# Optimization experiments

Hardware: AMD Instinct MI355X
Metric: run time of the kernel (lower is better)

## Reference

```python
import jax, jax.numpy as jnp
import numpy as np

D_MODEL = 1024
N_HEADS = 16
HEAD_DIM = D_MODEL // N_HEADS
WINDOW = 512


def _rope(q, k, seq_len, head_dim):
    # interleaved RoPE, identical to the torch implementation
    theta = 1.0 / 10000.0 ** (jnp.arange(0, head_dim, 2, dtype=jnp.float32) / head_dim)
    pos = jnp.arange(seq_len, dtype=jnp.float32)
    freqs = jnp.outer(pos, theta)                      # [S, hD/2]
    cos_f = jnp.cos(freqs)[None, None]                 # [1,1,S,hD/2]
    sin_f = jnp.sin(freqs)[None, None]

    def rotate(x):
        x1, x2 = x[..., ::2], x[..., 1::2]
        return jnp.stack([x1 * cos_f - x2 * sin_f, x1 * sin_f + x2 * cos_f], axis=-1).reshape(x.shape)

    return rotate(q), rotate(k)


def _sliding_window_attn(q, k, v, W, scale):
    # chunked O(S*W) causal sliding-window attention
    B, nH, S, hD = q.shape
    n_chunks = (S + W - 1) // W
    pad_s = n_chunks * W - S
    k_pad = jnp.pad(k, ((0, 0), (0, 0), (W, pad_s), (0, 0)))
    v_pad = jnp.pad(v, ((0, 0), (0, 0), (W, pad_s), (0, 0)))
    q_pad = jnp.pad(q, ((0, 0), (0, 0), (0, pad_s), (0, 0)))
    q_c = q_pad.reshape(B, nH, n_chunks, W, hD)
    k_r = k_pad.reshape(B, nH, n_chunks + 1, W, hD)
    v_r = v_pad.reshape(B, nH, n_chunks + 1, W, hD)
    # window i = chunks [i, i+1] of the left-padded sequence (== torch unfold)
    k_c = jnp.concatenate([k_r[:, :, :-1], k_r[:, :, 1:]], axis=3)  # [B,nH,C,2W,hD]
    v_c = jnp.concatenate([v_r[:, :, :-1], v_r[:, :, 1:]], axis=3)
    attn = jnp.einsum('bhcqd,bhckd->bhcqk', q_c, k_c) * scale

    qi = jnp.arange(W)[:, None]
    ki = jnp.arange(2 * W)[None, :]
    cw_mask = (ki <= qi) | (ki > qi + W)               # [W, 2W]
    chunk_idx = jnp.arange(n_chunks)[:, None]
    abs_k = chunk_idx * W + ki - W                     # [C, 2W]
    pad_mask = (abs_k < 0) | (abs_k >= S)
    q_pos = jnp.arange(n_chunks * W).reshape(n_chunks, W)
    full_mask = cw_mask[None] | pad_mask[:, None, :] | (q_pos >= S)[..., None]  # [C,W,2W]

    attn = jnp.where(full_mask[None, None], -jnp.inf, attn)
    attn = jax.nn.softmax(attn, axis=-1)
    attn = jnp.nan_to_num(attn, nan=0.0)
    out = jnp.einsum('bhcqk,bhckd->bhcqd', attn, v_c)
    return out.reshape(B, nH, n_chunks * W, hD)[:, :, :S]


def _rmsnorm(x, w):
    eps = jnp.finfo(x.dtype).eps
    return x * jax.lax.rsqrt(jnp.mean(x * x, axis=-1, keepdims=True) + eps) * w


def _sdpa(q, k, v, scale):
    s = jnp.einsum('bhqd,bhkd->bhqk', q, k) * scale
    return jnp.einsum('bhqk,bhkd->bhqd', jax.nn.softmax(s, axis=-1), v)


def setup_inputs() -> dict:
    key = jax.random.key(0)
    ks = jax.random.split(key, 11)
    D = D_MODEL
    std = 0.02
    return {
        'x': jax.random.normal(ks[0], (2, 4096, D), jnp.float32),
        'landmarks': jax.random.normal(ks[1], (2, 256, D), jnp.float32),
        'archived_landmarks': jax.random.normal(ks[2], (2, 128, D), jnp.float32),
        'W_qkv': jax.random.normal(ks[3], (D, 3 * D), jnp.float32) * std,
        'W_lm': jax.random.normal(ks[4], (D, 2 * D), jnp.float32) * std,
        'W_arch': jax.random.normal(ks[5], (D, 2 * D), jnp.float32) * std,
        'W_o': jax.random.normal(ks[6], (D, D), jnp.float32) * std,
        'W_gate': jax.random.normal(ks[7], (3 * D, 2 * D), jnp.float32) * std,
        'g_local': jnp.ones((D,), jnp.float32),
        'g_lm': jnp.ones((D,), jnp.float32),
        'g_arch': jnp.ones((D,), jnp.float32),
    }


def reference(x, landmarks, archived_landmarks, W_qkv, W_lm, W_arch, W_o, W_gate, g_local, g_lm, g_arch):
    B, S, D = x.shape
    nH, hD = N_HEADS, HEAD_DIM
    scale = hD ** -0.5

    def rsh(t, L):
        return jnp.transpose(t.reshape(B, L, nH, hD), (0, 2, 1, 3))

    q, k, v = jnp.split(x @ W_qkv, 3, axis=-1)
    Q, K, V = rsh(q, S), rsh(k, S), rsh(v, S)
    Q, K = _rope(Q, K, S, hD)

    Weff = min(WINDOW, S)
    out_loc = _sliding_window_attn(Q, K, V, Weff, scale)  # S > Weff -> chunked path
    out_loc = _rmsnorm(jnp.transpose(out_loc, (0, 2, 1, 3)).reshape(B, S, D), g_local)

    L = landmarks.shape[1]
    K_lm, V_lm = jnp.split(landmarks @ W_lm, 2, axis=-1)
    out_lm = _sdpa(Q, rsh(K_lm, L), rsh(V_lm, L), scale)
    out_lm = _rmsnorm(jnp.transpose(out_lm, (0, 2, 1, 3)).reshape(B, S, D), g_lm)

    A = archived_landmarks.shape[1]
    K_a, V_a = jnp.split(archived_landmarks @ W_arch, 2, axis=-1)
    out_a = _sdpa(Q, rsh(K_a, A), rsh(V_a, A), scale)
    out_a = _rmsnorm(jnp.transpose(out_a, (0, 2, 1, 3)).reshape(B, S, D), g_arch)

    concat = jnp.concatenate([out_loc, out_lm, out_a], axis=-1)
    gate, value = jnp.split(concat @ W_gate, 2, axis=-1)
    return (jax.nn.silu(gate) * value) @ W_o
```

## Files before the change

### kernel.cpp

```cpp
#include <hip/hip_runtime.h>
#include <cstdint>
#include <cstddef>

typedef __bf16 bf16;
typedef __bf16 bf16x2 __attribute__((ext_vector_type(2)));
typedef __bf16 bf16x4 __attribute__((ext_vector_type(4)));
typedef __bf16 bf16x8 __attribute__((ext_vector_type(8)));
typedef float  f32x2 __attribute__((ext_vector_type(2)));
typedef float  f32x4 __attribute__((ext_vector_type(4)));

#define DEVFN __device__ __forceinline__
#define BAR()  asm volatile("s_barrier" ::: "memory")
#define VMW0() asm volatile("s_waitcnt vmcnt(0)" ::: "memory")
#define VMW3() asm volatile("s_waitcnt vmcnt(3)" ::: "memory")
#define VMW4() asm volatile("s_waitcnt vmcnt(4)" ::: "memory")
#define MFMA16 __builtin_amdgcn_mfma_f32_16x16x32_bf16

DEVFN void gld_lds16(void* lds, const void* g) {
  __builtin_amdgcn_global_load_lds(
      (__attribute__((address_space(1))) void*)g,
      (__attribute__((address_space(3))) void*)lds,
      16, 0, 0);
}

__global__ void cast_f32_bf16(const float* __restrict__ in, bf16* __restrict__ out, int n4) {
  int i = blockIdx.x * blockDim.x + threadIdx.x;
  if (i < n4) {
    f32x4 v = reinterpret_cast<const f32x4*>(in)[i];
    bf16x4 o;
    o[0] = (bf16)v[0]; o[1] = (bf16)v[1]; o[2] = (bf16)v[2]; o[3] = (bf16)v[3];
    reinterpret_cast<bf16x4*>(out)[i] = o;
  }
}

__global__ void transpose_cast(const float* __restrict__ in, bf16* __restrict__ out,
                               int R, int C) {
  __shared__ float t[32][33];
  int tx = threadIdx.x, ty = threadIdx.y;
  int c = blockIdx.x * 32 + tx;
  #pragma unroll
  for (int j = 0; j < 4; ++j) {
    int r = blockIdx.y * 32 + ty + j * 8;
    t[ty + j * 8][tx] = in[(size_t)r * C + c];
  }
  __syncthreads();
  int rr = blockIdx.y * 32 + tx;
  #pragma unroll
  for (int j = 0; j < 4; ++j) {
    int cc = blockIdx.x * 32 + ty + j * 8;
    out[(size_t)cc * R + rr] = (bf16)t[tx][ty + j * 8];
  }
}

__global__ void rope_table(float* __restrict__ tab) {
  int idx = blockIdx.x * 256 + threadIdx.x;
  int s = idx >> 5, i = idx & 31;
  float theta = powf(10000.f, -(float)(2 * i) * (1.f / 64.f));
  float f = (float)s * theta;
  tab[idx * 2]     = cosf(f);
  tab[idx * 2 + 1] = sinf(f);
}

template<typename OT>
__global__ __launch_bounds__(512) void gemm256(
    const bf16* __restrict__ A, const bf16* __restrict__ Bt, OT* __restrict__ C,
    int M, int N, int K) {
  __shared__ alignas(16) bf16 lds[2][2][2][256 * 32];
  const int tid = threadIdx.x;
  const int w = tid >> 6, l = tid & 63;
  const int l15 = l & 15, lg = l >> 4;
  const int wm = w >> 2, wn = w & 3;
  const int nwg = gridDim.x, qx = nwg >> 3;
  const int swz = (blockIdx.x & 7) * qx + (blockIdx.x >> 3);
  const int gx = N >> 8;
  const int m0 = (swz / gx) << 8;
  const int n0 = (swz % gx) << 8;
  const int nt = K >> 6;

  auto stage = [&](int b, int ab, int kk, int t) {
    const bf16* __restrict__ src = ab ? Bt : A;
    const int base0 = ab ? n0 : m0;
    const int k0 = (t << 6) + (kk << 5);
    #pragma unroll
    for (int i = 0; i < 2; ++i) {
      int u = i * 512 + tid;
      int row = u >> 2, slot = u & 3;
      int sslot = slot ^ ((row >> 1) & 3);
      gld_lds16(&lds[b][ab][kk][(i * 512 + w * 64) * 8],
                src + (size_t)(base0 + row) * K + k0 + sslot * 8);
    }
  };
  auto rd = [&](int b, int ab, int kk, int r) -> bf16x8 {
    return *reinterpret_cast<const bf16x8*>(
        &lds[b][ab][kk][(r << 5) + ((lg ^ ((r >> 1) & 3)) << 3)]);
  };

  f32x4 acc[8][4] = {};
  bf16x8 aLo[4], aHi[4], bfr[4];

  stage(0, 0, 0, 0);
  stage(0, 1, 0, 0);
  stage(0, 0, 1, 0);
  stage(0, 1, 1, 0);
  VMW4();
  BAR();

  for (int t = 0; t < nt; ++t) {
    const int c = t & 1;
    const bool st = (t + 1) < nt;
    #pragma unroll
    for (int f = 0; f < 4; ++f) aLo[f] = rd(c, 0, 0, wm * 128 + f * 16 + l15);
    #pragma unroll
    for (int f = 0; f < 4; ++f) bfr[f] = rd(c, 1, 0, wn * 64 + f * 16 + l15);
    if (st) stage(c ^ 1, 0, 0, t + 1);
    BAR();
    __builtin_amdgcn_s_setprio(1);
    #pragma unroll
    for (int mi = 0; mi < 4; ++mi)
      #pragma unroll
      for (int ni = 0; ni < 4; ++ni)
        acc[mi][ni] = MFMA16(aLo[mi], bfr[ni], acc[mi][ni], 0, 0, 0);
    __builtin_amdgcn_s_setprio(0);
    #pragma unroll
    for (int f = 0; f < 4; ++f) aHi[f] = rd(c, 0, 0, wm * 128 + (f + 4) * 16 + l15);
    BAR();
    if (st) stage(c ^ 1, 1, 0, t + 1);
    BAR();
    __builtin_amdgcn_s_setprio(1);
    #pragma unroll
    for (int mi = 0; mi < 4; ++mi)
      #pragma unroll
      for (int ni = 0; ni < 4; ++ni)
        acc[mi + 4][ni] = MFMA16(aHi[mi], bfr[ni], acc[mi + 4][ni], 0, 0, 0);
    __builtin_amdgcn_s_setprio(0);
    if (st) { VMW4(); } else { VMW0(); }
    BAR();
    #pragma unroll
    for (int f = 0; f < 4; ++f) aLo[f] = rd(c, 0, 1, wm * 128 + f * 16 + l15);
    #pragma unroll
    for (int f = 0; f < 4; ++f) bfr[f] = rd(c, 1, 1, wn * 64 + f * 16 + l15);
    if (st) stage(c ^ 1, 0, 1, t + 1);
    BAR();
    __builtin_amdgcn_s_setprio(1);
    #pragma unroll
    for (int mi = 0; mi < 4; ++mi)
      #pragma unroll
      for (int ni = 0; ni < 4; ++ni)
        acc[mi][ni] = MFMA16(aLo[mi], bfr[ni], acc[mi][ni], 0, 0, 0);
    __builtin_amdgcn_s_setprio(0);
    #pragma unroll
    for (int f = 0; f < 4; ++f) aHi[f] = rd(c, 0, 1, wm * 128 + (f + 4) * 16 + l15);
    BAR();
    if (st) stage(c ^ 1, 1, 1, t + 1);
    BAR();
    __builtin_amdgcn_s_setprio(1);
    #pragma unroll
    for (int mi = 0; mi < 4; ++mi)
      #pragma unroll
      for (int ni = 0; ni < 4; ++ni)
        acc[mi + 4][ni] = MFMA16(aHi[mi], bfr[ni], acc[mi + 4][ni], 0, 0, 0);
    __builtin_amdgcn_s_setprio(0);
    VMW4();
    BAR();
  }

  #pragma unroll
  for (int mi = 0; mi < 8; ++mi) {
    #pragma unroll
    for (int r = 0; r < 4; ++r) {
      int row = m0 + wm * 128 + mi * 16 + lg * 4 + r;
      OT* crow = C + (size_t)row * N + n0 + wn * 64 + l15;
      #pragma unroll
      for (int ni = 0; ni < 4; ++ni) crow[ni * 16] = (OT)acc[mi][ni][r];
    }
  }
}

template<typename OT>
__global__ __launch_bounds__(512) void gemm256n128(
    const bf16* __restrict__ A, const bf16* __restrict__ Bt, OT* __restrict__ C,
    int M, int N, int K) {
  __shared__ alignas(16) bf16 ldsA[2][2][256 * 32];
  __shared__ alignas(16) bf16 ldsB[2][2][128 * 32];
  const int tid = threadIdx.x;
  const int w = tid >> 6, l = tid & 63;
  const int l15 = l & 15, lg = l >> 4;
  const int wm = w >> 1, wn = w & 1;
  const int nwg = gridDim.x, qx = nwg >> 3;
  const int swz = (blockIdx.x & 7) * qx + (blockIdx.x >> 3);
  const int gx = N >> 7;
  const int m0 = (swz / gx) << 8;
  const int n0 = (swz % gx) << 7;
  const int nt = K >> 6;

  auto stageA = [&](int b, int kk, int t) {
    const int k0 = (t << 6) + (kk << 5);
    #pragma unroll
    for (int i = 0; i < 2; ++i) {
      int u = i * 512 + tid;
      int row = u >> 2, slot = u & 3;
      int ss = slot ^ ((row >> 1) & 3);
      gld_lds16(&ldsA[b][kk][(i * 512 + w * 64) * 8],
                A + (size_t)(m0 + row) * K + k0 + ss * 8);
    }
  };
  auto stageB = [&](int b, int kk, int t) {
    const int k0 = (t << 6) + (kk << 5);
    int row = tid >> 2, slot = tid & 3;
    int ss = slot ^ ((row >> 1) & 3);
    gld_lds16(&ldsB[b][kk][(w * 64) * 8],
              Bt + (size_t)(n0 + row) * K + k0 + ss * 8);
  };
  auto rdA = [&](int b, int kk, int r) -> bf16x8 {
    return *reinterpret_cast<const bf16x8*>(
        &ldsA[b][kk][(r << 5) + ((lg ^ ((r >> 1) & 3)) << 3)]);
  };
  auto rdB = [&](int b, int kk, int r) -> bf16x8 {
    return *reinterpret_cast<const bf16x8*>(
        &ldsB[b][kk][(r << 5) + ((lg ^ ((r >> 1) & 3)) << 3)]);
  };

  f32x4 acc[4][4] = {};
  bf16x8 af[4], bf[4];

  stageA(0, 0, 0); stageB(0, 0, 0);
  stageA(0, 1, 0); stageB(0, 1, 0);
  VMW3();
  BAR();

  for (int t = 0; t < nt; ++t) {
    const int c = t & 1;
    const bool st = (t + 1) < nt;
    #pragma unroll
    for (int kk = 0; kk < 2; ++kk) {
      #pragma unroll
      for (int f = 0; f < 4; ++f) af[f] = rdA(c, kk, wm * 64 + f * 16 + l15);
      #pragma unroll
      for (int f = 0; f < 4; ++f) bf[f] = rdB(c, kk, wn * 64 + f * 16 + l15);
      if (st) { stageA(c ^ 1, kk, t + 1); stageB(c ^ 1, kk, t + 1); }
      BAR();
      __builtin_amdgcn_s_setprio(1);
      #pragma unroll
      for (int mi = 0; mi < 4; ++mi)
        #pragma unroll
        for (int ni = 0; ni < 4; ++ni)
          acc[mi][ni] = MFMA16(af[mi], bf[ni], acc[mi][ni], 0, 0, 0);
      __builtin_amdgcn_s_setprio(0);
      if (st) { VMW3(); }
      else if (kk == 0) { VMW0(); }
      BAR();
    }
  }

  #pragma unroll
  for (int mi = 0; mi < 4; ++mi) {
    #pragma unroll
    for (int r = 0; r < 4; ++r) {
      int row = m0 + wm * 64 + mi * 16 + lg * 4 + r;
      OT* crow = C + (size_t)row * N + n0 + wn * 64 + l15;
      #pragma unroll
      for (int ni = 0; ni < 4; ++ni) crow[ni * 16] = (OT)acc[mi][ni][r];
    }
  }
}

template<typename OT>
__global__ __launch_bounds__(256) void gemm_bf16(
    const bf16* __restrict__ A, const bf16* __restrict__ Bt, OT* __restrict__ C,
    int M, int N, int K) {
  __shared__ alignas(16) bf16 As[128 * 64];
  __shared__ alignas(16) bf16 Bs[128 * 64];
  int tid = threadIdx.x;
  int w = tid >> 6, l = tid & 63;
  int l15 = l & 15, lg = l >> 4;
  int m0 = blockIdx.y * 128;
  int n0 = blockIdx.x * 128;
  int wr = (w >> 1) * 64, wc = (w & 1) * 64;
  f32x4 acc[4][4] = {};
  const size_t aBase = (size_t)m0 * K;
  const size_t bBase = (size_t)n0 * K;
  int nk = K >> 6;
  for (int kt = 0; kt < nk; ++kt) {
    int k0 = kt << 6;
    #pragma unroll
    for (int it = 0; it < 4; ++it) {
      int c = it * 256 + tid;
      int row = c >> 3, c8 = c & 7;
      gld_lds16(&As[(size_t)(it * 256 + w * 64) * 8],
                A + aBase + (size_t)row * K + k0 + c8 * 8);
      gld_lds16(&Bs[(size_t)(it * 256 + w * 64) * 8],
                Bt + bBase + (size_t)row * K + k0 + c8 * 8);
    }
    __syncthreads();
    #pragma unroll
    for (int kk = 0; kk < 64; kk += 32) {
      bf16x8 a[4], b[4];
      #pragma unroll
      for (int i = 0; i < 4; ++i)
        a[i] = *reinterpret_cast<const bf16x8*>(&As[(wr + i * 16 + l15) * 64 + kk + lg * 8]);
      #pragma unroll
      for (int i = 0; i < 4; ++i)
        b[i] = *reinterpret_cast<const bf16x8*>(&Bs[(wc + i * 16 + l15) * 64 + kk + lg * 8]);
      #pragma unroll
      for (int mi = 0; mi < 4; ++mi)
        #pragma unroll
        for (int ni = 0; ni < 4; ++ni)
          acc[mi][ni] = MFMA16(a[mi], b[ni], acc[mi][ni], 0, 0, 0);
    }
    __syncthreads();
  }
  #pragma unroll
  for (int mi = 0; mi < 4; ++mi) {
    #pragma unroll
    for (int r = 0; r < 4; ++r) {
      int row = m0 + wr + mi * 16 + lg * 4 + r;
      OT* crow = C + (size_t)row * N + n0 + wc + l15;
      #pragma unroll
      for (int ni = 0; ni < 4; ++ni) crow[ni * 16] = (OT)acc[mi][ni][r];
    }
  }
}

__global__ void rope_qk(const bf16* __restrict__ qkv, const float* __restrict__ tab,
                        bf16* __restrict__ Qb, bf16* __restrict__ Kb) {
  int idx = blockIdx.x * 256 + threadIdx.x;
  int i = idx & 31;
  int h = (idx >> 5) & 15;
  int bs = idx >> 9;
  int s = bs & 4095;
  int b = bs >> 12;
  const bf16* row = qkv + (size_t)bs * 3072;
  bf16x2 q2 = *reinterpret_cast<const bf16x2*>(row + h * 64 + 2 * i);
  bf16x2 k2 = *reinterpret_cast<const bf16x2*>(row + 1024 + h * 64 + 2 * i);
  f32x2 cs = *reinterpret_cast<const f32x2*>(tab + s * 64 + 2 * i);
  float c = cs[0], sn = cs[1];
  float q0 = (float)q2[0], q1 = (float)q2[1];
  float k0 = (float)k2[0], k1 = (float)k2[1];
  size_t ob = (((size_t)(b * 16 + h) * 4096) + s) * 64 + 2 * i;
  bf16x2 qo, ko;
  qo[0] = (bf16)((q0 * c - q1 * sn) * 0.125f);
  qo[1] = (bf16)((q0 * sn + q1 * c) * 0.125f);
  ko[0] = (bf16)(k0 * c - k1 * sn);
  ko[1] = (bf16)(k0 * sn + k1 * c);
  *reinterpret_cast<bf16x2*>(Qb + ob) = qo;
  *reinterpret_cast<bf16x2*>(Kb + ob) = ko;
}

__global__ void kv_post(const bf16* __restrict__ kv, bf16* __restrict__ Kdst,
                        bf16* __restrict__ Vt, int Lk, int rs, int koff, int voff) {
  __shared__ float t[64][65];
  int s0 = blockIdx.x * 64;
  int h = blockIdx.y, b = blockIdx.z;
  int tid = threadIdx.x;
  int lane_d = tid & 63;
  int rq = tid >> 6;
  const bf16* base = kv + (size_t)b * Lk * rs;
  if (Kdst) {
    #pragma unroll
    for (int r = 0; r < 16; ++r) {
      int si = r * 4 + rq;
      Kdst[(((size_t)(b * 16 + h) * Lk) + s0 + si) * 64 + lane_d] =
          base[(size_t)(s0 + si) * rs + koff + h * 64 + lane_d];
    }
  }
  #pragma unroll
  for (int r = 0; r < 16; ++r) {
    int si = r * 4 + rq;
    t[si][lane_d] = (float)base[(size_t)(s0 + si) * rs + voff + h * 64 + lane_d];
  }
  __syncthreads();
  #pragma unroll
  for (int r = 0; r < 16; ++r) {
    int d = r * 4 + rq;
    Vt[(((size_t)(b * 16 + h) * 64) + d) * Lk + s0 + lane_d] = (bf16)t[lane_d][d];
  }
}

__global__ __launch_bounds__(256) void attn_win(
    const bf16* __restrict__ Qb, const bf16* __restrict__ Kb,
    const bf16* __restrict__ Vt, bf16* __restrict__ outc) {
  constexpr int S = 4096;
  __shared__ alignas(16) bf16 Ks[2][64 * 64];
  __shared__ alignas(16) bf16 Vs[2][64 * 64];
  __shared__ alignas(16) bf16 Ps[4][2][16 * 72];
  const int tid = threadIdx.x;
  const int w = tid >> 6, l = tid & 63;
  const int l15 = l & 15, lg = l >> 4;
  const int h = blockIdx.y, b = blockIdx.z;
  const int Q0 = blockIdx.x * 128;
  const int qt0 = Q0 >> 6;

  const bf16* Kbase = Kb + ((size_t)(b * 16 + h) * S) * 64;
  const bf16* Vbase = Vt + ((size_t)(b * 16 + h) * 64) * S;

  bf16x8 qf[2][2];
  #pragma unroll
  for (int c = 0; c < 2; ++c) {
    size_t qrow = (((size_t)(b * 16 + h) * S) + Q0 + w * 32 + c * 16 + l15) * 64;
    qf[c][0] = *reinterpret_cast<const bf16x8*>(Qb + qrow + lg * 8);
    qf[c][1] = *reinterpret_cast<const bf16x8*>(Qb + qrow + 32 + lg * 8);
  }

  const int kt_hi = qt0 + 1;
  const int kt_lo = qt0 >= 8 ? qt0 - 8 : 0;

  auto stage = [&](int buf, int kt) {
    const bf16* kg = Kbase + (size_t)kt * 64 * 64;
    #pragma unroll
    for (int it = 0; it < 2; ++it) {
      int u = it * 256 + tid;
      int row = u >> 3, sl = u & 7;
      gld_lds16(&Ks[buf][(it * 256 + w * 64) * 8], kg + row * 64 + (sl ^ (row & 7)) * 8);
    }
    #pragma unroll
    for (int it = 0; it < 2; ++it) {
      int u = it * 256 + tid;
      int row = u >> 3, sl = u & 7;
      gld_lds16(&Vs[buf][(it * 256 + w * 64) * 8],
                Vbase + (size_t)row * S + kt * 64 + (sl ^ (row & 7)) * 8);
    }
  };

  float mrow[2] = {-30000.f, -30000.f}, lsum[2] = {0.f, 0.f};
  f32x4 acc[2][4] = {};

  stage(0, kt_hi);

  int i = 0;
  for (int kt = kt_hi; kt >= kt_lo; --kt, ++i) {
    const int buf = i & 1;
    if (kt > kt_lo) { stage(buf ^ 1, kt - 1); VMW4(); } else { VMW0(); }
    BAR();

    f32x4 st[2][4] = {};
    #pragma unroll
    for (int kk = 0; kk < 2; ++kk) {
      #pragma unroll
      for (int f = 0; f < 4; ++f) {
        bf16x8 kf = *reinterpret_cast<const bf16x8*>(
            &Ks[buf][(f * 16 + l15) * 64 + (((kk * 4 + lg) ^ (l15 & 7)) << 3)]);
        #pragma unroll
        for (int c = 0; c < 2; ++c)
          st[c][f] = MFMA16(kf, qf[c][kk], st[c][f], 0, 0, 0);
      }
    }

    if (kt >= qt0) {
      #pragma unroll
      for (int c = 0; c < 2; ++c) {
        int q = Q0 + w * 32 + c * 16 + l15;
        #pragma unroll
        for (int f = 0; f < 4; ++f)
          #pragma unroll
          for (int r = 0; r < 4; ++r)
            if (kt * 64 + f * 16 + lg * 4 + r > q) st[c][f][r] = -1e30f;
      }
    }
    if (kt <= qt0 - 7) {
      #pragma unroll
      for (int c = 0; c < 2; ++c) {
        int q = Q0 + w * 32 + c * 16 + l15;
        #pragma unroll
        for (int f = 0; f < 4; ++f)
          #pragma unroll
          for (int r = 0; r < 4; ++r)
            if (kt * 64 + f * 16 + lg * 4 + r <= q - 512) st[c][f][r] = -1e30f;
      }
    }

    #pragma unroll
    for (int c = 0; c < 2; ++c) {
      float rm = -1e30f;
      #pragma unroll
      for (int f = 0; f < 4; ++f)
        #pragma unroll
        for (int r = 0; r < 4; ++r) rm = fmaxf(rm, st[c][f][r]);
      rm = fmaxf(rm, __shfl_xor(rm, 16));
      rm = fmaxf(rm, __shfl_xor(rm, 32));
      float mnew = fmaxf(mrow[c], rm);
      float fsc = __expf(mrow[c] - mnew);
      float ps = 0.f;
      #pragma unroll
      for (int f = 0; f < 4; ++f) {
        bf16x4 pv;
        #pragma unroll
        for (int r = 0; r < 4; ++r) {
          float p = __expf(st[c][f][r] - mnew);
          ps += p;
          pv[r] = (bf16)p;
        }
        *reinterpret_cast<bf16x4*>(&Ps[w][c][l15 * 72 + f * 16 + lg * 4]) = pv;
      }
      ps += __shfl_xor(ps, 16);
      ps += __shfl_xor(ps, 32);
      lsum[c] = lsum[c] * fsc + ps;
      mrow[c] = mnew;
      #pragma unroll
      for (int r = 0; r < 4; ++r) {
        float fr = __shfl(fsc, lg * 4 + r);
        #pragma unroll
        for (int f = 0; f < 4; ++f) acc[c][f][r] *= fr;
      }
    }

    #pragma unroll
    for (int kk = 0; kk < 2; ++kk) {
      bf16x8 pa[2];
      #pragma unroll
      for (int c = 0; c < 2; ++c)
        pa[c] = *reinterpret_cast<const bf16x8*>(&Ps[w][c][l15 * 72 + kk * 32 + lg * 8]);
      #pragma unroll
      for (int f = 0; f < 4; ++f) {
        bf16x8 vf = *reinterpret_cast<const bf16x8*>(
            &Vs[buf][(f * 16 + l15) * 64 + (((kk * 4 + lg) ^ (l15 & 7)) << 3)]);
        #pragma unroll
        for (int c = 0; c < 2; ++c)
          acc[c][f] = MFMA16(pa[c], vf, acc[c][f], 0, 0, 0);
      }
    }
    BAR();
  }

  #pragma unroll
  for (int c = 0; c < 2; ++c) {
    float inv = 1.f / lsum[c];
    #pragma unroll
    for (int r = 0; r < 4; ++r) {
      float ir = __shfl(inv, lg * 4 + r);
      int srow = Q0 + w * 32 + c * 16 + lg * 4 + r;
      bf16* orow = outc + ((size_t)b * S + srow) * 3072 + h * 64 + l15;
      #pragma unroll
      for (int f = 0; f < 4; ++f) orow[f * 16] = (bf16)(acc[c][f][r] * ir);
    }
  }
}

template<int LKV, int NQI>
__global__ __launch_bounds__(512) void attn_res(
    const bf16* __restrict__ Qb, const bf16* __restrict__ Kb,
    const bf16* __restrict__ Vt, bf16* __restrict__ outc, int col_off) {
  constexpr int S = 4096;
  __shared__ alignas(16) bf16 Ks[LKV * 64];
  __shared__ alignas(16) bf16 Vs[64 * LKV];
  __shared__ alignas(16) bf16 Ps[8][2][16 * 72];
  const int tid = threadIdx.x;
  const int w = tid >> 6, l = tid & 63;
  const int l15 = l & 15, lg = l >> 4;
  const int h = blockIdx.y, b = blockIdx.z;
  const bf16* Kg = Kb + ((size_t)(b * 16 + h) * LKV) * 64;
  const bf16* Vg = Vt + ((size_t)(b * 16 + h) * 64) * LKV;

  constexpr int NU = LKV / 64;
  constexpr int SPR = LKV / 8;
  #pragma unroll
  for (int i = 0; i < NU; ++i) {
    int u = i * 512 + tid;
    int row = u >> 3, sl = u & 7;
    gld_lds16(&Ks[(i * 512 + w * 64) * 8], Kg + row * 64 + (sl ^ (row & 7)) * 8);
  }
  #pragma unroll
  for (int i = 0; i < NU; ++i) {
    int u = i * 512 + tid;
    int row = u / SPR, sl = u % SPR;
    gld_lds16(&Vs[(i * 512 + w * 64) * 8],
              Vg + (size_t)row * LKV + ((sl & ~7) + ((sl & 7) ^ (row & 7))) * 8);
  }
  __syncthreads();

  for (int qi = 0; qi < NQI; ++qi) {
    const int Q0 = (blockIdx.x * NQI + qi) * 256 + w * 32;
    bf16x8 qf[2][2];
    #pragma unroll
    for (int c = 0; c < 2; ++c) {
      size_t qrow = (((size_t)(b * 16 + h) * S) + Q0 + c * 16 + l15) * 64;
      qf[c][0] = *reinterpret_cast<const bf16x8*>(Qb + qrow + lg * 8);
      qf[c][1] = *reinterpret_cast<const bf16x8*>(Qb + qrow + 32 + lg * 8);
    }
    float mrow[2] = {-30000.f, -30000.f}, lsum[2] = {0.f, 0.f};
    f32x4 acc[2][4] = {};

    #pragma unroll
    for (int kt = 0; kt < LKV / 64; ++kt) {
      f32x4 st[2][4] = {};
      #pragma unroll
      for (int kk = 0; kk < 2; ++kk) {
        #pragma unroll
        for (int f = 0; f < 4; ++f) {
          bf16x8 kf = *reinterpret_cast<const bf16x8*>(
              &Ks[(kt * 64 + f * 16 + l15) * 64 + (((kk * 4 + lg) ^ (l15 & 7)) << 3)]);
          #pragma unroll
          for (int c = 0; c < 2; ++c)
            st[c][f] = MFMA16(kf, qf[c][kk], st[c][f], 0, 0, 0);
        }
      }
      #pragma unroll
      for (int c = 0; c < 2; ++c) {
        float rm = -1e30f;
        #pragma unroll
        for (int f = 0; f < 4; ++f)
          #pragma unroll
          for (int r = 0; r < 4; ++r) rm = fmaxf(rm, st[c][f][r]);
        rm = fmaxf(rm, __shfl_xor(rm, 16));
        rm = fmaxf(rm, __shfl_xor(rm, 32));
        float mnew = fmaxf(mrow[c], rm);
        float fsc = __expf(mrow[c] - mnew);
        float ps = 0.f;
        #pragma unroll
        for (int f = 0; f < 4; ++f) {
          bf16x4 pv;
          #pragma unroll
          for (int r = 0; r < 4; ++r) {
            float p = __expf(st[c][f][r] - mnew);
            ps += p;
            pv[r] = (bf16)p;
          }
          *reinterpret_cast<bf16x4*>(&Ps[w][c][l15 * 72 + f * 16 + lg * 4]) = pv;
        }
        ps += __shfl_xor(ps, 16);
        ps += __shfl_xor(ps, 32);
        lsum[c] = lsum[c] * fsc + ps;
        mrow[c] = mnew;
        #pragma unroll
        for (int r = 0; r < 4; ++r) {
          float fr = __shfl(fsc, lg * 4 + r);
          #pragma unroll
          for (int f = 0; f < 4; ++f) acc[c][f][r] *= fr;
        }
      }
      #pragma unroll
      for (int kk = 0; kk < 2; ++kk) {
        bf16x8 pa[2];
        #pragma unroll
        for (int c = 0; c < 2; ++c)
          pa[c] = *reinterpret_cast<const bf16x8*>(&Ps[w][c][l15 * 72 + kk * 32 + lg * 8]);
        #pragma unroll
        for (int f = 0; f < 4; ++f) {
          bf16x8 vf = *reinterpret_cast<const bf16x8*>(
              &Vs[(f * 16 + l15) * LKV + ((kt * 8 + ((kk * 4 + lg) ^ (l15 & 7))) << 3)]);
          #pragma unroll
          for (int c = 0; c < 2; ++c)
            acc[c][f] = MFMA16(pa[c], vf, acc[c][f], 0, 0, 0);
        }
      }
    }

    #pragma unroll
    for (int c = 0; c < 2; ++c) {
      float inv = 1.f / lsum[c];
      #pragma unroll
      for (int r = 0; r < 4; ++r) {
        float ir = __shfl(inv, lg * 4 + r);
        int srow = Q0 + c * 16 + lg * 4 + r;
        bf16* orow = outc + ((size_t)b * S + srow) * 3072 + col_off + h * 64 + l15;
        #pragma unroll
        for (int f = 0; f < 4; ++f) orow[f * 16] = (bf16)(acc[c][f][r] * ir);
      }
    }
  }
}

__global__ __launch_bounds__(256) void rmsnorm_kernel(
    bf16* data, const float* __restrict__ g0,
    const float* __restrict__ g1, const float* __restrict__ g2) {
  int token = blockIdx.x;
  int seg = blockIdx.y;
  const float* g = seg == 0 ? g0 : (seg == 1 ? g1 : g2);
  int tid = threadIdx.x;
  size_t base = (size_t)token * 3072 + seg * 1024;
  bf16x4 bv = reinterpret_cast<const bf16x4*>(data + base)[tid];
  f32x4 v;
  #pragma unroll
  for (int j = 0; j < 4; ++j) v[j] = (float)bv[j];
  float ss = v[0] * v[0] + v[1] * v[1] + v[2] * v[2] + v[3] * v[3];
  #pragma unroll
  for (int m = 1; m < 64; m <<= 1) ss += __shfl_xor(ss, m);
  __shared__ float red[4];
  if ((tid & 63) == 0) red[tid >> 6] = ss;
  __syncthreads();
  float tot = red[0] + red[1] + red[2] + red[3];
  float sc = rsqrtf(tot * (1.f / 1024.f) + 1.19209290e-07f);
  f32x4 gv = reinterpret_cast<const f32x4*>(g)[tid];
  bf16x4 o;
  #pragma unroll
  for (int j = 0; j < 4; ++j) o[j] = (bf16)(v[j] * sc * gv[j]);
  reinterpret_cast<bf16x4*>(data + base)[tid] = o;
}

__global__ void silu_kernel(const bf16* __restrict__ gv, bf16* __restrict__ out) {
  int T = blockIdx.x * 256 + threadIdx.x;
  int row = T >> 8, c4 = (T & 255) * 4;
  bf16x4 g = *reinterpret_cast<const bf16x4*>(gv + (size_t)row * 2048 + c4);
  bf16x4 vv = *reinterpret_cast<const bf16x4*>(gv + (size_t)row * 2048 + 1024 + c4);
  bf16x4 o;
  #pragma unroll
  for (int j = 0; j < 4; ++j) {
    float x = (float)g[j];
    o[j] = (bf16)((x / (1.f + __expf(-x))) * (float)vv[j]);
  }
  *reinterpret_cast<bf16x4*>(out + (size_t)row * 1024 + c4) = o;
}

extern "C" void kernel_launch(void* const* d_in, const int* in_sizes, int n_in,
                              void* d_out, int out_size, void* d_ws, size_t ws_size,
                              hipStream_t stream) {
  (void)in_sizes; (void)n_in; (void)out_size; (void)ws_size;
  const float* x       = (const float*)d_in[0];
  const float* lm      = (const float*)d_in[1];
  const float* arch    = (const float*)d_in[2];
  const float* W_qkv   = (const float*)d_in[3];
  const float* W_lm    = (const float*)d_in[4];
  const float* W_arch  = (const float*)d_in[5];
  const float* W_o     = (const float*)d_in[6];
  const float* W_gate  = (const float*)d_in[7];
  const float* g_local = (const float*)d_in[8];
  const float* g_lm    = (const float*)d_in[9];
  const float* g_arch  = (const float*)d_in[10];
  float* out = (float*)d_out;

  char* ws = (char*)d_ws;
  size_t off = 0;
  auto alloc = [&](size_t bytes) -> void* {
    void* p = ws + off;
    off += (bytes + 255) & ~(size_t)255;
    return p;
  };
  bf16*  Wqkv_t   = (bf16*) alloc(3072ull * 1024 * 2);
  bf16*  Wlm_t    = (bf16*) alloc(2048ull * 1024 * 2);
  bf16*  Warch_t  = (bf16*) alloc(2048ull * 1024 * 2);
  bf16*  Wgate_t  = (bf16*) alloc(2048ull * 3072 * 2);
  bf16*  Wo_t     = (bf16*) alloc(1024ull * 1024 * 2);
  bf16*  lm_bf    = (bf16*) alloc(512ull * 1024 * 2);
  bf16*  arch_bf  = (bf16*) alloc(256ull * 1024 * 2);
  float* ropetab  = (float*)alloc(4096ull * 64 * 4);
  bf16*  Klm      = (bf16*) alloc(2ull * 16 * 256 * 64 * 2);
  bf16*  Vlm_t    = (bf16*) alloc(2ull * 16 * 64 * 256 * 2);
  bf16*  Ka       = (bf16*) alloc(2ull * 16 * 128 * 64 * 2);
  bf16*  Va_t     = (bf16*) alloc(2ull * 16 * 64 * 128 * 2);
  bf16*  lmkv_bf  = (bf16*) alloc(512ull * 2048 * 2);
  bf16*  akv_bf   = (bf16*) alloc(256ull * 2048 * 2);
  char* R1 = (char*)alloc(8192ull * 1024 * 2);
  bf16* x_bf  = (bf16*)R1;
  bf16* gated = (bf16*)R1;
  char* R2 = (char*)alloc(8192ull * 3072 * 2);
  bf16* qkv_bf  = (bf16*)R2;
  bf16* concatb = (bf16*)R2;
  char* R3 = (char*)alloc(3ull * 16 * 1024 * 1024);
  bf16* Qb = (bf16*)R3;
  bf16* Kb = (bf16*)(R3 + 16ull * 1024 * 1024);
  bf16* Vt = (bf16*)(R3 + 32ull * 1024 * 1024);
  bf16* gv = (bf16*)R3;

  transpose_cast<<<dim3(96, 32), dim3(32, 8), 0, stream>>>(W_qkv, Wqkv_t, 1024, 3072);
  transpose_cast<<<dim3(64, 32), dim3(32, 8), 0, stream>>>(W_lm, Wlm_t, 1024, 2048);
  transpose_cast<<<dim3(64, 32), dim3(32, 8), 0, stream>>>(W_arch, Warch_t, 1024, 2048);
  transpose_cast<<<dim3(64, 96), dim3(32, 8), 0, stream>>>(W_gate, Wgate_t, 3072, 2048);
  transpose_cast<<<dim3(32, 32), dim3(32, 8), 0, stream>>>(W_o, Wo_t, 1024, 1024);
  cast_f32_bf16<<<8192, 256, 0, stream>>>(x, x_bf, 8192 * 1024 / 4);
  cast_f32_bf16<<<512, 256, 0, stream>>>(lm, lm_bf, 512 * 1024 / 4);
  cast_f32_bf16<<<256, 256, 0, stream>>>(arch, arch_bf, 256 * 1024 / 4);
  rope_table<<<512, 256, 0, stream>>>(ropetab);

  gemm256n128<bf16><<<32 * 24, 512, 0, stream>>>(x_bf, Wqkv_t, qkv_bf, 8192, 3072, 1024);
  gemm_bf16<bf16><<<dim3(16, 4), 256, 0, stream>>>(lm_bf, Wlm_t, lmkv_bf, 512, 2048, 1024);
  gemm_bf16<bf16><<<dim3(16, 2), 256, 0, stream>>>(arch_bf, Warch_t, akv_bf, 256, 2048, 1024);

  rope_qk<<<16384, 256, 0, stream>>>(qkv_bf, ropetab, Qb, Kb);
  kv_post<<<dim3(64, 16, 2), 256, 0, stream>>>(qkv_bf, nullptr, Vt, 4096, 3072, 0, 2048);
  kv_post<<<dim3(4, 16, 2), 256, 0, stream>>>(lmkv_bf, Klm, Vlm_t, 256, 2048, 0, 1024);
  kv_post<<<dim3(2, 16, 2), 256, 0, stream>>>(akv_bf, Ka, Va_t, 128, 2048, 0, 1024);

  attn_win<<<dim3(32, 16, 2), 256, 0, stream>>>(Qb, Kb, Vt, concatb);
  attn_res<256, 2><<<dim3(8, 16, 2), 512, 0, stream>>>(Qb, Klm, Vlm_t, concatb, 1024);
  attn_res<128, 2><<<dim3(8, 16, 2), 512, 0, stream>>>(Qb, Ka, Va_t, concatb, 2048);

  rmsnorm_kernel<<<dim3(8192, 3), 256, 0, stream>>>(concatb, g_local, g_lm, g_arch);

  gemm256<bf16><<<32 * 8, 512, 0, stream>>>(concatb, Wgate_t, gv, 8192, 2048, 3072);
  silu_kernel<<<8192, 256, 0, stream>>>(gv, gated);
  gemm256n128<float><<<32 * 8, 512, 0, stream>>>(gated, Wo_t, out, 8192, 1024, 1024);
}
```

Before: 448.0 us.

## Fuse SiLU gating into gate GEMM, deepen GEMM pipeline, shrink attention tiles

The gate GEMM now interleaves gate and value columns of W_gate inside each tile and applies SiLU(gate)*value in the epilogue. This removes the separate silu kernel and the round trip of the intermediate through global memory. Both GEMMs switch to a 4-buffer, 32-wide-K pipeline that keeps three stages in flight with fewer barriers per step. The sliding-window attention kernel processes 64 queries per block instead of 128, doubling the grid and tightening the mask checks. In exchange the GEMMs use more LDS and the attention kernel loads each K/V tile for half as many queries.

```diff
diff --git a/kernel.cpp b/kernel.cpp
--- a/kernel.cpp
+++ b/kernel.cpp
@@ -14,6 +14,8 @@
 #define VMW0() asm volatile("s_waitcnt vmcnt(0)" ::: "memory")
 #define VMW3() asm volatile("s_waitcnt vmcnt(3)" ::: "memory")
 #define VMW4() asm volatile("s_waitcnt vmcnt(4)" ::: "memory")
+#define VMW6() asm volatile("s_waitcnt vmcnt(6)" ::: "memory")
+#define VMW8() asm volatile("s_waitcnt vmcnt(8)" ::: "memory")
 #define MFMA16 __builtin_amdgcn_mfma_f32_16x16x32_bf16
 
 DEVFN void gld_lds16(void* lds, const void* g) {
@@ -61,58 +63,67 @@
   tab[idx * 2 + 1] = sinf(f);
 }
 
-template<typename OT>
-__global__ __launch_bounds__(512) void gemm256(
-    const bf16* __restrict__ A, const bf16* __restrict__ Bt, OT* __restrict__ C,
-    int M, int N, int K) {
-  __shared__ alignas(16) bf16 lds[2][2][2][256 * 32];
+__global__ __launch_bounds__(512) void gemm_gate(
+    const bf16* __restrict__ A, const bf16* __restrict__ Bt,
+    bf16* __restrict__ G, int K) {
+  __shared__ alignas(16) bf16 ldsA[4][256 * 32];
+  __shared__ alignas(16) bf16 ldsB[4][256 * 32];
   const int tid = threadIdx.x;
   const int w = tid >> 6, l = tid & 63;
   const int l15 = l & 15, lg = l >> 4;
   const int wm = w >> 2, wn = w & 3;
   const int nwg = gridDim.x, qx = nwg >> 3;
   const int swz = (blockIdx.x & 7) * qx + (blockIdx.x >> 3);
-  const int gx = N >> 8;
-  const int m0 = (swz / gx) << 8;
-  const int n0 = (swz % gx) << 8;
-  const int nt = K >> 6;
-
-  auto stage = [&](int b, int ab, int kk, int t) {
-    const bf16* __restrict__ src = ab ? Bt : A;
-    const int base0 = ab ? n0 : m0;
-    const int k0 = (t << 6) + (kk << 5);
+  const int m0 = (swz >> 3) << 8;
+  const int n0 = (swz & 7) << 7;
+  const int ns = K >> 5;
+
+  auto stage = [&](int s) {
+    const int buf = s & 3;
+    const int k0 = s << 5;
     #pragma unroll
     for (int i = 0; i < 2; ++i) {
       int u = i * 512 + tid;
       int row = u >> 2, slot = u & 3;
-      int sslot = slot ^ ((row >> 1) & 3);
-      gld_lds16(&lds[b][ab][kk][(i * 512 + w * 64) * 8],
-                src + (size_t)(base0 + row) * K + k0 + sslot * 8);
+      int ss = slot ^ ((row >> 1) & 3);
+      gld_lds16(&ldsA[buf][(i * 512 + w * 64) * 8],
+                A + (size_t)(m0 + row) * K + k0 + ss * 8);
+    }
+    #pragma unroll
+    for (int i = 0; i < 2; ++i) {
+      int u = i * 512 + tid;
+      int row = u >> 2, slot = u & 3;
+      int ss = slot ^ ((row >> 1) & 3);
+      int q = row >> 6, o = row & 63;
+      int grow = (o < 32) ? (n0 + q * 32 + o) : (1024 + n0 + q * 32 + o - 32);
+      gld_lds16(&ldsB[buf][(i * 512 + w * 64) * 8],
+                Bt + (size_t)grow * K + k0 + ss * 8);
     }
   };
-  auto rd = [&](int b, int ab, int kk, int r) -> bf16x8 {
+  auto rdA = [&](int buf, int r) -> bf16x8 {
     return *reinterpret_cast<const bf16x8*>(
-        &lds[b][ab][kk][(r << 5) + ((lg ^ ((r >> 1) & 3)) << 3)]);
+        &ldsA[buf][(r << 5) + ((lg ^ ((r >> 1) & 3)) << 3)]);
   };
+  auto rdB = [&](int buf, int r) -> bf16x8 {
+    return *reinterpret_cast<const bf16x8*>(
+        &ldsB[buf][(r << 5) + ((lg ^ ((r >> 1) & 3)) << 3)]);
+  };
 
   f32x4 acc[8][4] = {};
-  bf16x8 aLo[4], aHi[4], bfr[4];
-
-  stage(0, 0, 0, 0);
-  stage(0, 1, 0, 0);
-  stage(0, 0, 1, 0);
-  stage(0, 1, 1, 0);
-  VMW4();
+
+  stage(0); stage(1); stage(2);
+  VMW8();
   BAR();
 
-  for (int t = 0; t < nt; ++t) {
-    const int c = t & 1;
-    const bool st = (t + 1) < nt;
-    #pragma unroll
-    for (int f = 0; f < 4; ++f) aLo[f] = rd(c, 0, 0, wm * 128 + f * 16 + l15);
-    #pragma unroll
-    for (int f = 0; f < 4; ++f) bfr[f] = rd(c, 1, 0, wn * 64 + f * 16 + l15);
-    if (st) stage(c ^ 1, 0, 0, t + 1);
+  for (int s = 0; s < ns; ++s) {
+    const int c = s & 3;
+    bf16x8 aLo[4], aHi[4], bfr[4];
+    #pragma unroll
+    for (int f = 0; f < 4; ++f) aLo[f] = rdA(c, wm * 128 + f * 16 + l15);
+    #pragma unroll
+    for (int f = 0; f < 4; ++f) bfr[f] = rdB(c, wn * 64 + f * 16 + l15);
+    const bool st3 = (s + 3) < ns;
+    if (st3) stage(s + 3);
     BAR();
     __builtin_amdgcn_s_setprio(1);
     #pragma unroll
@@ -122,10 +133,7 @@
         acc[mi][ni] = MFMA16(aLo[mi], bfr[ni], acc[mi][ni], 0, 0, 0);
     __builtin_amdgcn_s_setprio(0);
     #pragma unroll
-    for (int f = 0; f < 4; ++f) aHi[f] = rd(c, 0, 0, wm * 128 + (f + 4) * 16 + l15);
-    BAR();
-    if (st) stage(c ^ 1, 1, 0, t + 1);
-    BAR();
+    for (int f = 0; f < 4; ++f) aHi[f] = rdA(c, wm * 128 + (f + 4) * 16 + l15);
     __builtin_amdgcn_s_setprio(1);
     #pragma unroll
     for (int mi = 0; mi < 4; ++mi)
@@ -133,34 +141,10 @@
       for (int ni = 0; ni < 4; ++ni)
         acc[mi + 4][ni] = MFMA16(aHi[mi], bfr[ni], acc[mi + 4][ni], 0, 0, 0);
     __builtin_amdgcn_s_setprio(0);
-    if (st) { VMW4(); } else { VMW0(); }
-    BAR();
-    #pragma unroll
-    for (int f = 0; f < 4; ++f) aLo[f] = rd(c, 0, 1, wm * 128 + f * 16 + l15);
-    #pragma unroll
-    for (int f = 0; f < 4; ++f) bfr[f] = rd(c, 1, 1, wn * 64 + f * 16 + l15);
-    if (st) stage(c ^ 1, 0, 1, t + 1);
-    BAR();
-    __builtin_amdgcn_s_setprio(1);
-    #pragma unroll
-    for (int mi = 0; mi < 4; ++mi)
-      #pragma unroll
-      for (int ni = 0; ni < 4; ++ni)
-        acc[mi][ni] = MFMA16(aLo[mi], bfr[ni], acc[mi][ni], 0, 0, 0);
-    __builtin_amdgcn_s_setprio(0);
-    #pragma unroll
-    for (int f = 0; f < 4; ++f) aHi[f] = rd(c, 0, 1, wm * 128 + (f + 4) * 16 + l15);
-    BAR();
-    if (st) stage(c ^ 1, 1, 1, t + 1);
-    BAR();
-    __builtin_amdgcn_s_setprio(1);
-    #pragma unroll
-    for (int mi = 0; mi < 4; ++mi)
-      #pragma unroll
-      for (int ni = 0; ni < 4; ++ni)
-        acc[mi + 4][ni] = MFMA16(aHi[mi], bfr[ni], acc[mi + 4][ni], 0, 0, 0);
-    __builtin_amdgcn_s_setprio(0);
-    VMW4();
+    const int rem = ns - 1 - s;
+    if (st3) { VMW8(); }
+    else if (rem == 2) { VMW4(); }
+    else if (rem == 1) { VMW0(); }
     BAR();
   }
 
@@ -169,19 +153,22 @@
     #pragma unroll
     for (int r = 0; r < 4; ++r) {
       int row = m0 + wm * 128 + mi * 16 + lg * 4 + r;
-      OT* crow = C + (size_t)row * N + n0 + wn * 64 + l15;
-      #pragma unroll
-      for (int ni = 0; ni < 4; ++ni) crow[ni * 16] = (OT)acc[mi][ni][r];
+      bf16* grow = G + (size_t)row * 1024 + n0 + wn * 32 + l15;
+      #pragma unroll
+      for (int ni = 0; ni < 2; ++ni) {
+        float g = acc[mi][ni][r], v = acc[mi][ni + 2][r];
+        grow[ni * 16] = (bf16)((g / (1.f + __expf(-g))) * v);
+      }
     }
   }
 }
 
 template<typename OT>
-__global__ __launch_bounds__(512) void gemm256n128(
+__global__ __launch_bounds__(512) void gemmK128(
     const bf16* __restrict__ A, const bf16* __restrict__ Bt, OT* __restrict__ C,
-    int M, int N, int K) {
-  __shared__ alignas(16) bf16 ldsA[2][2][256 * 32];
-  __shared__ alignas(16) bf16 ldsB[2][2][128 * 32];
+    int N, int K) {
+  __shared__ alignas(16) bf16 ldsA[4][256 * 32];
+  __shared__ alignas(16) bf16 ldsB[4][128 * 32];
   const int tid = threadIdx.x;
   const int w = tid >> 6, l = tid & 63;
   const int l15 = l & 15, lg = l >> 4;
@@ -191,65 +178,63 @@
   const int gx = N >> 7;
   const int m0 = (swz / gx) << 8;
   const int n0 = (swz % gx) << 7;
-  const int nt = K >> 6;
-
-  auto stageA = [&](int b, int kk, int t) {
-    const int k0 = (t << 6) + (kk << 5);
+  const int ns = K >> 5;
+
+  auto stage = [&](int s) {
+    const int buf = s & 3;
+    const int k0 = s << 5;
     #pragma unroll
     for (int i = 0; i < 2; ++i) {
       int u = i * 512 + tid;
       int row = u >> 2, slot = u & 3;
       int ss = slot ^ ((row >> 1) & 3);
-      gld_lds16(&ldsA[b][kk][(i * 512 + w * 64) * 8],
+      gld_lds16(&ldsA[buf][(i * 512 + w * 64) * 8],
                 A + (size_t)(m0 + row) * K + k0 + ss * 8);
     }
+    {
+      int row = tid >> 2, slot = tid & 3;
+      int ss = slot ^ ((row >> 1) & 3);
+      gld_lds16(&ldsB[buf][(w * 64) * 8],
+                Bt + (size_t)(n0 + row) * K + k0 + ss * 8);
+    }
   };
-  auto stageB = [&](int b, int kk, int t) {
-    const int k0 = (t << 6) + (kk << 5);
-    int row = tid >> 2, slot = tid & 3;
-    int ss = slot ^ ((row >> 1) & 3);
-    gld_lds16(&ldsB[b][kk][(w * 64) * 8],
-              Bt + (size_t)(n0 + row) * K + k0 + ss * 8);
+  auto rdA = [&](int buf, int r) -> bf16x8 {
+    return *reinterpret_cast<const bf16x8*>(
+        &ldsA[buf][(r << 5) + ((lg ^ ((r >> 1) & 3)) << 3)]);
   };
-  auto rdA = [&](int b, int kk, int r) -> bf16x8 {
+  auto rdB = [&](int buf, int r) -> bf16x8 {
     return *reinterpret_cast<const bf16x8*>(
-        &ldsA[b][kk][(r << 5) + ((lg ^ ((r >> 1) & 3)) << 3)]);
+        &ldsB[buf][(r << 5) + ((lg ^ ((r >> 1) & 3)) << 3)]);
   };
-  auto rdB = [&](int b, int kk, int r) -> bf16x8 {
-    return *reinterpret_cast<const bf16x8*>(
-        &ldsB[b][kk][(r << 5) + ((lg ^ ((r >> 1) & 3)) << 3)]);
-  };
 
   f32x4 acc[4][4] = {};
-  bf16x8 af[4], bf[4];
-
-  stageA(0, 0, 0); stageB(0, 0, 0);
-  stageA(0, 1, 0); stageB(0, 1, 0);
-  VMW3();
+
+  stage(0); stage(1); stage(2);
+  VMW6();
   BAR();
 
-  for (int t = 0; t < nt; ++t) {
-    const int c = t & 1;
-    const bool st = (t + 1) < nt;
-    #pragma unroll
-    for (int kk = 0; kk < 2; ++kk) {
-      #pragma unroll
-      for (int f = 0; f < 4; ++f) af[f] = rdA(c, kk, wm * 64 + f * 16 + l15);
-      #pragma unroll
-      for (int f = 0; f < 4; ++f) bf[f] = rdB(c, kk, wn * 64 + f * 16 + l15);
-      if (st) { stageA(c ^ 1, kk, t + 1); stageB(c ^ 1, kk, t + 1); }
-      BAR();
-      __builtin_amdgcn_s_setprio(1);
-      #pragma unroll
-      for (int mi = 0; mi < 4; ++mi)
-        #pragma unroll
-        for (int ni = 0; ni < 4; ++ni)
-          acc[mi][ni] = MFMA16(af[mi], bf[ni], acc[mi][ni], 0, 0, 0);
-      __builtin_amdgcn_s_setprio(0);
-      if (st) { VMW3(); }
-      else if (kk == 0) { VMW0(); }
-      BAR();
-    }
+  for (int s = 0; s < ns; ++s) {
+    const int c = s & 3;
+    bf16x8 af[4], bf[4];
+    #pragma unroll
+    for (int f = 0; f < 4; ++f) af[f] = rdA(c, wm * 64 + f * 16 + l15);
+    #pragma unroll
+    for (int f = 0; f < 4; ++f) bf[f] = rdB(c, wn * 64 + f * 16 + l15);
+    const bool st3 = (s + 3) < ns;
+    if (st3) stage(s + 3);
+    BAR();
+    __builtin_amdgcn_s_setprio(1);
+    #pragma unroll
+    for (int mi = 0; mi < 4; ++mi)
+      #pragma unroll
+      for (int ni = 0; ni < 4; ++ni)
+        acc[mi][ni] = MFMA16(af[mi], bf[ni], acc[mi][ni], 0, 0, 0);
+    __builtin_amdgcn_s_setprio(0);
+    const int rem = ns - 1 - s;
+    if (st3) { VMW6(); }
+    else if (rem == 2) { VMW3(); }
+    else if (rem == 1) { VMW0(); }
+    BAR();
   }
 
   #pragma unroll
@@ -376,33 +361,30 @@
   }
 }
 
-__global__ __launch_bounds__(256) void attn_win(
+__global__ __launch_bounds__(256) void attn64(
     const bf16* __restrict__ Qb, const bf16* __restrict__ Kb,
     const bf16* __restrict__ Vt, bf16* __restrict__ outc) {
   constexpr int S = 4096;
   __shared__ alignas(16) bf16 Ks[2][64 * 64];
   __shared__ alignas(16) bf16 Vs[2][64 * 64];
-  __shared__ alignas(16) bf16 Ps[4][2][16 * 72];
-  const int tid = threadIdx.x;
-  const int w = tid >> 6, l = tid & 63;
-  const int l15 = l & 15, lg = l >> 4;
-  const int h = blockIdx.y, b = blockIdx.z;
-  const int Q0 = blockIdx.x * 128;
-  const int qt0 = Q0 >> 6;
-
+  __shared__ alignas(16) bf16 Ps[4][16 * 72];
+  int tid = threadIdx.x;
+  int w = tid >> 6, l = tid & 63;
+  int l15 = l & 15, lg = l >> 4;
+  int qt = blockIdx.x, h = blockIdx.y, b = blockIdx.z;
+
+  size_t qrow = (((size_t)(b * 16 + h) * S) + qt * 64 + w * 16 + l15) * 64;
+  bf16x8 qf[2];
+  qf[0] = *reinterpret_cast<const bf16x8*>(Qb + qrow + lg * 8);
+  qf[1] = *reinterpret_cast<const bf16x8*>(Qb + qrow + 32 + lg * 8);
   const bf16* Kbase = Kb + ((size_t)(b * 16 + h) * S) * 64;
   const bf16* Vbase = Vt + ((size_t)(b * 16 + h) * 64) * S;
 
-  bf16x8 qf[2][2];
-  #pragma unroll
-  for (int c = 0; c < 2; ++c) {
-    size_t qrow = (((size_t)(b * 16 + h) * S) + Q0 + w * 32 + c * 16 + l15) * 64;
-    qf[c][0] = *reinterpret_cast<const bf16x8*>(Qb + qrow + lg * 8);
-    qf[c][1] = *reinterpret_cast<const bf16x8*>(Qb + qrow + 32 + lg * 8);
-  }
-
-  const int kt_hi = qt0 + 1;
-  const int kt_lo = qt0 >= 8 ? qt0 - 8 : 0;
+  float mrow = -1e30f, lsum = 0.f;
+  f32x4 acc[4] = {};
+
+  const int kt_hi = qt;
+  const int kt_lo = qt >= 8 ? qt - 8 : 0;
 
   auto stage = [&](int buf, int kt) {
     const bf16* kg = Kbase + (size_t)kt * 64 * 64;
@@ -421,9 +403,6 @@
     }
   };
 
-  float mrow[2] = {-30000.f, -30000.f}, lsum[2] = {0.f, 0.f};
-  f32x4 acc[2][4] = {};
-
   stage(0, kt_hi);
 
   int i = 0;
@@ -432,106 +411,86 @@
     if (kt > kt_lo) { stage(buf ^ 1, kt - 1); VMW4(); } else { VMW0(); }
     BAR();
 
-    f32x4 st[2][4] = {};
+    f32x4 st[4] = {};
     #pragma unroll
     for (int kk = 0; kk < 2; ++kk) {
       #pragma unroll
       for (int f = 0; f < 4; ++f) {
         bf16x8 kf = *reinterpret_cast<const bf16x8*>(
             &Ks[buf][(f * 16 + l15) * 64 + (((kk * 4 + lg) ^ (l15 & 7)) << 3)]);
-        #pragma unroll
-        for (int c = 0; c < 2; ++c)
-          st[c][f] = MFMA16(kf, qf[c][kk], st[c][f], 0, 0, 0);
+        st[f] = MFMA16(kf, qf[kk], st[f], 0, 0, 0);
       }
     }
 
-    if (kt >= qt0) {
-      #pragma unroll
-      for (int c = 0; c < 2; ++c) {
-        int q = Q0 + w * 32 + c * 16 + l15;
-        #pragma unroll
-        for (int f = 0; f < 4; ++f)
-          #pragma unroll
-          for (int r = 0; r < 4; ++r)
-            if (kt * 64 + f * 16 + lg * 4 + r > q) st[c][f][r] = -1e30f;
+    int qi = w * 16 + l15;
+    if (kt == qt) {
+      #pragma unroll
+      for (int f = 0; f < 4; ++f)
+        #pragma unroll
+        for (int r = 0; r < 4; ++r)
+          if (f * 16 + lg * 4 + r > qi) st[f][r] = -1e30f;
+    } else if (kt == qt - 8) {
+      #pragma unroll
+      for (int f = 0; f < 4; ++f)
+        #pragma unroll
+        for (int r = 0; r < 4; ++r)
+          if (f * 16 + lg * 4 + r <= qi) st[f][r] = -1e30f;
+    }
+
+    float rm = -1e30f;
+    #pragma unroll
+    for (int f = 0; f < 4; ++f)
+      #pragma unroll
+      for (int r = 0; r < 4; ++r) rm = fmaxf(rm, st[f][r]);
+    rm = fmaxf(rm, __shfl_xor(rm, 16));
+    rm = fmaxf(rm, __shfl_xor(rm, 32));
+    float mnew = fmaxf(mrow, rm);
+    float fsc = __expf(mrow - mnew);
+    float ps = 0.f;
+    #pragma unroll
+    for (int f = 0; f < 4; ++f) {
+      bf16x4 pv;
+      #pragma unroll
+      for (int r = 0; r < 4; ++r) {
+        float p = __expf(st[f][r] - mnew);
+        ps += p;
+        pv[r] = (bf16)p;
       }
-    }
-    if (kt <= qt0 - 7) {
-      #pragma unroll
-      for (int c = 0; c < 2; ++c) {
-        int q = Q0 + w * 32 + c * 16 + l15;
-        #pragma unroll
-        for (int f = 0; f < 4; ++f)
-          #pragma unroll
-          for (int r = 0; r < 4; ++r)
-            if (kt * 64 + f * 16 + lg * 4 + r <= q - 512) st[c][f][r] = -1e30f;
-      }
-    }
-
-    #pragma unroll
-    for (int c = 0; c < 2; ++c) {
-      float rm = -1e30f;
-      #pragma unroll
-      for (int f = 0; f < 4; ++f)
-        #pragma unroll
-        for (int r = 0; r < 4; ++r) rm = fmaxf(rm, st[c][f][r]);
-      rm = fmaxf(rm, __shfl_xor(rm, 16));
-      rm = fmaxf(rm, __shfl_xor(rm, 32));
-      float mnew = fmaxf(mrow[c], rm);
-      float fsc = __expf(mrow[c] - mnew);
-      float ps = 0.f;
-      #pragma unroll
-      for (int f = 0; f < 4; ++f) {
-        bf16x4 pv;
-        #pragma unroll
-        for (int r = 0; r < 4; ++r) {
-          float p = __expf(st[c][f][r] - mnew);
-          ps += p;
-          pv[r] = (bf16)p;
-        }
-        *reinterpret_cast<bf16x4*>(&Ps[w][c][l15 * 72 + f * 16 + lg * 4]) = pv;
-      }
-      ps += __shfl_xor(ps, 16);
-      ps += __shfl_xor(ps, 32);
-      lsum[c] = lsum[c] * fsc + ps;
-      mrow[c] = mnew;
-      #pragma unroll
-      for (int r = 0; r < 4; ++r) {
-        float fr = __shfl(fsc, lg * 4 + r);
-        #pragma unroll
-        for (int f = 0; f < 4; ++f) acc[c][f][r] *= fr;
-      }
+      *reinterpret_cast<bf16x4*>(&Ps[w][l15 * 72 + f * 16 + lg * 4]) = pv;
+    }
+    ps += __shfl_xor(ps, 16);
+    ps += __shfl_xor(ps, 32);
+    lsum = lsum * fsc + ps;
+    mrow = mnew;
+
+    #pragma unroll
+    for (int r = 0; r < 4; ++r) {
+      float fr = __shfl(fsc, lg * 4 + r);
+      #pragma unroll
+      for (int f = 0; f < 4; ++f) acc[f][r] *= fr;
     }
 
     #pragma unroll
     for (int kk = 0; kk < 2; ++kk) {
-      bf16x8 pa[2];
-      #pragma unroll
-      for (int c = 0; c < 2; ++c)
-        pa[c] = *reinterpret_cast<const bf16x8*>(&Ps[w][c][l15 * 72 + kk * 32 + lg * 8]);
+      bf16x8 pa = *reinterpret_cast<const bf16x8*>(&Ps[w][l15 * 72 + kk * 32 + lg * 8]);
       #pragma unroll
       for (int f = 0; f < 4; ++f) {
         bf16x8 vf = *reinterpret_cast<const bf16x8*>(
             &Vs[buf][(f * 16 + l15) * 64 + (((kk * 4 + lg) ^ (l15 & 7)) << 3)]);
-        #pragma unroll
-        for (int c = 0; c < 2; ++c)
-          acc[c][f] = MFMA16(pa[c], vf, acc[c][f], 0, 0, 0);
+        acc[f] = MFMA16(pa, vf, acc[f], 0, 0, 0);
       }
     }
     BAR();
   }
 
-  #pragma unroll
-  for (int c = 0; c < 2; ++c) {
-    float inv = 1.f / lsum[c];
-    #pragma unroll
-    for (int r = 0; r < 4; ++r) {
-      float ir = __shfl(inv, lg * 4 + r);
-      int srow = Q0 + w * 32 + c * 16 + lg * 4 + r;
-      bf16* orow = outc + ((size_t)b * S + srow) * 3072 + h * 64 + l15;
-      #pragma unroll
-      for (int f = 0; f < 4; ++f) orow[f * 16] = (bf16)(acc[c][f][r] * ir);
-    }
+  float inv = 1.f / lsum;
+  #pragma unroll
+  for (int r = 0; r < 4; ++r) {
+    float ir = __shfl(inv, lg * 4 + r);
+    int srow = qt * 64 + w * 16 + lg * 4 + r;
+    bf16* orow = outc + ((size_t)b * S + srow) * 3072 + h * 64 + l15;
+    #pragma unroll
+    for (int f = 0; f < 4; ++f) orow[f * 16] = (bf16)(acc[f][r] * ir);
   }
 }
 
@@ -684,20 +643,6 @@
   #pragma unroll
   for (int j = 0; j < 4; ++j) o[j] = (bf16)(v[j] * sc * gv[j]);
   reinterpret_cast<bf16x4*>(data + base)[tid] = o;
-}
-
-__global__ void silu_kernel(const bf16* __restrict__ gv, bf16* __restrict__ out) {
-  int T = blockIdx.x * 256 + threadIdx.x;
-  int row = T >> 8, c4 = (T & 255) * 4;
-  bf16x4 g = *reinterpret_cast<const bf16x4*>(gv + (size_t)row * 2048 + c4);
-  bf16x4 vv = *reinterpret_cast<const bf16x4*>(gv + (size_t)row * 2048 + 1024 + c4);
-  bf16x4 o;
-  #pragma unroll
-  for (int j = 0; j < 4; ++j) {
-    float x = (float)g[j];
-    o[j] = (bf16)((x / (1.f + __expf(-x))) * (float)vv[j]);
-  }
-  *reinterpret_cast<bf16x4*>(out + (size_t)row * 1024 + c4) = o;
 }
 
 extern "C" void kernel_launch(void* const* d_in, const int* in_sizes, int n_in,
@@ -748,7 +693,6 @@
   bf16* Qb = (bf16*)R3;
   bf16* Kb = (bf16*)(R3 + 16ull * 1024 * 1024);
   bf16* Vt = (bf16*)(R3 + 32ull * 1024 * 1024);
-  bf16* gv = (bf16*)R3;
 
   transpose_cast<<<dim3(96, 32), dim3(32, 8), 0, stream>>>(W_qkv, Wqkv_t, 1024, 3072);
   transpose_cast<<<dim3(64, 32), dim3(32, 8), 0, stream>>>(W_lm, Wlm_t, 1024, 2048);
@@ -760,7 +704,7 @@
   cast_f32_bf16<<<256, 256, 0, stream>>>(arch, arch_bf, 256 * 1024 / 4);
   rope_table<<<512, 256, 0, stream>>>(ropetab);
 
-  gemm256n128<bf16><<<32 * 24, 512, 0, stream>>>(x_bf, Wqkv_t, qkv_bf, 8192, 3072, 1024);
+  gemmK128<bf16><<<768, 512, 0, stream>>>(x_bf, Wqkv_t, qkv_bf, 3072, 1024);
   gemm_bf16<bf16><<<dim3(16, 4), 256, 0, stream>>>(lm_bf, Wlm_t, lmkv_bf, 512, 2048, 1024);
   gemm_bf16<bf16><<<dim3(16, 2), 256, 0, stream>>>(arch_bf, Warch_t, akv_bf, 256, 2048, 1024);
 
@@ -769,13 +713,12 @@
   kv_post<<<dim3(4, 16, 2), 256, 0, stream>>>(lmkv_bf, Klm, Vlm_t, 256, 2048, 0, 1024);
   kv_post<<<dim3(2, 16, 2), 256, 0, stream>>>(akv_bf, Ka, Va_t, 128, 2048, 0, 1024);
 
-  attn_win<<<dim3(32, 16, 2), 256, 0, stream>>>(Qb, Kb, Vt, concatb);
+  attn64<<<dim3(64, 16, 2), 256, 0, stream>>>(Qb, Kb, Vt, concatb);
   attn_res<256, 2><<<dim3(8, 16, 2), 512, 0, stream>>>(Qb, Klm, Vlm_t, concatb, 1024);
   attn_res<128, 2><<<dim3(8, 16, 2), 512, 0, stream>>>(Qb, Ka, Va_t, concatb, 2048);
 
   rmsnorm_kernel<<<dim3(8192, 3), 256, 0, stream>>>(concatb, g_local, g_lm, g_arch);
 
-  gemm256<bf16><<<32 * 8, 512, 0, stream>>>(concatb, Wgate_t, gv, 8192, 2048, 3072);
-  silu_kernel<<<8192, 256, 0, stream>>>(gv, gated);
-  gemm256n128<float><<<32 * 8, 512, 0, stream>>>(gated, Wo_t, out, 8192, 1024, 1024);
-}
+  gemm_gate<<<256, 512, 0, stream>>>(concatb, Wgate_t, gated, 3072);
+  gemmK128<float><<<256, 512, 0, stream>>>(gated, Wo_t, out, 1024, 1024);
+}
```

After: 441.3 us. About the same (-1.5%).
